# Kernel optimization log

Hardware: AMD Instinct MI355X
Metric: run time of the kernel (lower is better)

The kernel has to match this reference:

```python
import jax, jax.numpy as jnp
import numpy as np

B, N, C, H, W = 16, 10, 128, 48, 48

def setup_inputs() -> dict:
    key = jax.random.key(0)
    k0, k1 = jax.random.split(key, 2)
    x = jax.random.normal(k0, (B, N, C, H, W), dtype=jnp.float32)
    # trainable interpolation params, initialized to 0.5 as in the torch module
    pos_dec = jnp.full((N,), 0.5, dtype=jnp.float32)
    length_dec = jnp.full((N,), 0.5, dtype=jnp.float32)
    # 1x1 conv == channel-mixing matmul over N*C channels
    NC = N * C
    conv_w = jax.random.normal(k1, (NC, NC), dtype=jnp.float32) * (1.0 / np.sqrt(NC))
    conv_b = jnp.zeros((NC,), dtype=jnp.float32)
    return {"x": x, "pos_dec": pos_dec, "length_dec": length_dec,
            "conv_w": conv_w, "conv_b": conv_b}


def reference(x, pos_dec, length_dec, conv_w, conv_b):
    b, n, c, h, w = x.shape
    d = c * h * w
    q = x.reshape(b, n, d)          # proj_query (B,N,CHW)
    k = q                           # proj_key has the same flattened features
    # bi_interpolate with pos_int=i, length_int=1 reduces in closed form to:
    #   s0 = (1-pd)*K[i]   + pd*K[i+1]                      (key_short row)
    #   s1 = ld*((1-pd)*K[i+1] + pd*K[i+2])                 (zero-padded short mixed with key_long)
    # where indices wrap mod N (key was concatenated with itself).
    idx = jnp.arange(n)
    k1_ = k[:, (idx + 1) % n]       # (B,N,D)
    k2_ = k[:, (idx + 2) % n]
    pd = pos_dec[None, :, None]
    ld = length_dec[None, :, None]
    s0 = (1.0 - pd) * k + pd * k1_
    s1 = ld * ((1.0 - pd) * k1_ + pd * k2_)
    S = jnp.stack([s0, s1], axis=2)                 # (B,N,2,D) interpolated keys per group
    logits = jnp.einsum('bnd,bnkd->bnk', q, S)      # per-group 2-way attention scores
    attn = jax.nn.softmax(logits, axis=-1)          # softmax over the 2 searched keys
    out = jnp.einsum('bnk,bnkd->bnd', attn, S)      # (B,N,D)
    feat = out.reshape(b, n * c, h, w)
    conv = jnp.einsum('oc,bchw->bohw', conv_w, feat) + conv_b[None, :, None, None]
    return conv + x.reshape(b, n * c, h, w)
```

## Files before the change

kernel.cpp:

```cpp
#include <hip/hip_runtime.h>
#include <hip/hip_bf16.h>

#define BB 16
#define NN 10
#define CC 128
#define HWD 2304
#define DD (CC*HWD)
#define NC (NN*CC)

#define CHP 72

#define BM 256
#define BN 256
#define BK 64
#define TK (NC/BK)

typedef __bf16 bf16x8 __attribute__((ext_vector_type(8)));
typedef float  f32x4  __attribute__((ext_vector_type(4)));
typedef float  f32x16 __attribute__((ext_vector_type(16)));

#define XT_BYTES ((size_t)BB*HWD*NC*2)
#define W2_BYTES ((size_t)BB*NC*NC*2)
#define PART_FLOATS (BB*NN*CHP*3)
#define HEAD ((size_t)262144)

__device__ __forceinline__ ushort f2bf(float f) {
    __hip_bfloat16 h = __float2bfloat16(f);
    return *reinterpret_cast<ushort*>(&h);
}

__device__ __forceinline__ void gload_lds16(const ushort* g, ushort* l) {
    __builtin_amdgcn_global_load_lds(
        (const __attribute__((address_space(1))) void*)(const void*)g,
        (__attribute__((address_space(3))) void*)(void*)l,
        16, 0, 0);
}

__global__ __launch_bounds__(256) void k_trans(const float* __restrict__ x,
                                               ushort* __restrict__ xT,
                                               float* __restrict__ part) {
    __shared__ float tile[32*129];
    __shared__ float red[4][3];
    int hwt = blockIdx.x;
    int b   = blockIdx.y;
    int t = threadIdx.x;
    int hw0 = hwt*32;
    const float* xb = x + (size_t)b*NN*DD;

    int c_[4], ch_[4];
    size_t off_[4];
    #pragma unroll
    for (int i = 0; i < 4; ++i) {
        int s = i*256 + t;
        c_[i] = s >> 3; ch_[i] = s & 7;
        off_[i] = (size_t)c_[i]*HWD + hw0 + ch_[i]*4;
    }

    float4 s0[4], s1[4], s2[4], s3[4];
    #pragma unroll
    for (int i = 0; i < 4; ++i) s0[i] = *(const float4*)(xb + (size_t)0*DD + off_[i]);
    #pragma unroll
    for (int i = 0; i < 4; ++i) s1[i] = *(const float4*)(xb + (size_t)1*DD + off_[i]);
    #pragma unroll
    for (int i = 0; i < 4; ++i) s2[i] = *(const float4*)(xb + (size_t)2*DD + off_[i]);

    int w = t >> 6, l = t & 63;

    for (int n = 0; n < NN; ++n) {
        int n3 = (n + 3) % NN;
        #pragma unroll
        for (int i = 0; i < 4; ++i) s3[i] = *(const float4*)(xb + (size_t)n3*DD + off_[i]);

        float d0 = 0.f, d1 = 0.f, d2 = 0.f;
        #pragma unroll
        for (int i = 0; i < 4; ++i) {
            d0 += s0[i].x*s0[i].x + s0[i].y*s0[i].y + s0[i].z*s0[i].z + s0[i].w*s0[i].w;
            d1 += s0[i].x*s1[i].x + s0[i].y*s1[i].y + s0[i].z*s1[i].z + s0[i].w*s1[i].w;
            d2 += s0[i].x*s2[i].x + s0[i].y*s2[i].y + s0[i].z*s2[i].z + s0[i].w*s2[i].w;
        }
        for (int o = 32; o > 0; o >>= 1) {
            d0 += __shfl_down(d0, o);
            d1 += __shfl_down(d1, o);
            d2 += __shfl_down(d2, o);
        }
        if (l == 0) { red[w][0] = d0; red[w][1] = d1; red[w][2] = d2; }

        #pragma unroll
        for (int i = 0; i < 4; ++i) {
            int hwb = ch_[i]*4, cc = c_[i];
            tile[(hwb+0)*129 + cc] = s0[i].x;
            tile[(hwb+1)*129 + cc] = s0[i].y;
            tile[(hwb+2)*129 + cc] = s0[i].z;
            tile[(hwb+3)*129 + cc] = s0[i].w;
        }
        __syncthreads();

        if (t == 0) {
            float r0 = 0.f, r1 = 0.f, r2 = 0.f;
            #pragma unroll
            for (int i = 0; i < 4; ++i) { r0 += red[i][0]; r1 += red[i][1]; r2 += red[i][2]; }
            float* o = part + ((size_t)(b*NN + n)*CHP + hwt)*3;
            o[0] = r0; o[1] = r1; o[2] = r2;
        }

        int hwl = t >> 4;
        int cc0 = (t & 15) * 8;
        #pragma unroll
        for (int p = 0; p < 2; ++p) {
            int hw = p*16 + hwl;
            const float* src = &tile[hw*129 + cc0];
            union { ushort us[8]; uint4 v; } pk;
            #pragma unroll
            for (int j = 0; j < 8; ++j) pk.us[j] = f2bf(src[j]);
            ushort* dst = xT + (size_t)b*HWD*NC + (size_t)(hw0 + hw)*NC + n*CC + cc0;
            *(uint4*)dst = pk.v;
        }
        __syncthreads();
        #pragma unroll
        for (int i = 0; i < 4; ++i) { s0[i] = s1[i]; s1[i] = s2[i]; s2[i] = s3[i]; }
    }
}

__global__ void k_coef(const float* __restrict__ part,
                       const float* __restrict__ pos_dec,
                       const float* __restrict__ len_dec,
                       float* __restrict__ coef) {
    int bn = threadIdx.x;
    if (bn >= BB*NN) return;
    int n = bn % NN;
    float d0 = 0.f, d1 = 0.f, d2 = 0.f;
    const float* p = part + (size_t)bn*CHP*3;
    for (int i = 0; i < CHP; ++i) { d0 += p[i*3]; d1 += p[i*3+1]; d2 += p[i*3+2]; }
    float pd = pos_dec[n], ld = len_dec[n];
    float l0 = (1.f - pd)*d0 + pd*d1;
    float l1 = ld*((1.f - pd)*d1 + pd*d2);
    float m  = fmaxf(l0, l1);
    float e0 = expf(l0 - m), e1 = expf(l1 - m);
    float inv = 1.f/(e0 + e1);
    float a0 = e0*inv, a1 = e1*inv;
    coef[bn*3+0] = a0*(1.f - pd);
    coef[bn*3+1] = a0*pd + a1*ld*(1.f - pd);
    coef[bn*3+2] = a1*ld*pd;
}

__global__ __launch_bounds__(256) void k_w2(const float* __restrict__ w,
                                            const float* __restrict__ coef,
                                            ushort* __restrict__ w2) {
    int b = blockIdx.y;
    size_t eid = ((size_t)blockIdx.x*256 + threadIdx.x)*8;
    int o  = (int)(eid / NC);
    int mc = (int)(eid % NC);
    int m = mc >> 7, c = mc & 127;
    int m1 = (m + 9) % 10, m2 = (m + 8) % 10;
    float c0 = coef[(b*NN + m )*3 + 0];
    float c1 = coef[(b*NN + m1)*3 + 1];
    float c2 = coef[(b*NN + m2)*3 + 2];
    const float* wr = w + (size_t)o*NC;
    float4 a0 = *(const float4*)(wr + m *128 + c);
    float4 a1 = *(const float4*)(wr + m *128 + c + 4);
    float4 u0 = *(const float4*)(wr + m1*128 + c);
    float4 u1 = *(const float4*)(wr + m1*128 + c + 4);
    float4 v0 = *(const float4*)(wr + m2*128 + c);
    float4 v1 = *(const float4*)(wr + m2*128 + c + 4);
    union { ushort us[8]; uint4 v; } pk;
    pk.us[0] = f2bf(c0*a0.x + c1*u0.x + c2*v0.x);
    pk.us[1] = f2bf(c0*a0.y + c1*u0.y + c2*v0.y);
    pk.us[2] = f2bf(c0*a0.z + c1*u0.z + c2*v0.z);
    pk.us[3] = f2bf(c0*a0.w + c1*u0.w + c2*v0.w);
    pk.us[4] = f2bf(c0*a1.x + c1*u1.x + c2*v1.x);
    pk.us[5] = f2bf(c0*a1.y + c1*u1.y + c2*v1.y);
    pk.us[6] = f2bf(c0*a1.z + c1*u1.z + c2*v1.z);
    pk.us[7] = f2bf(c0*a1.w + c1*u1.w + c2*v1.w);
    *(uint4*)(w2 + (size_t)b*NC*NC + eid) = pk.v;
}

__global__ __launch_bounds__(256) void k_wconv(const float* __restrict__ w,
                                               ushort* __restrict__ wb) {
    int i = blockIdx.x*blockDim.x + threadIdx.x;
    size_t idx = (size_t)i*4;
    if (idx >= (size_t)NC*NC) return;
    float4 a = *(const float4*)(w + idx);
    ushort4 o;
    o.x = f2bf(a.x); o.y = f2bf(a.y); o.z = f2bf(a.z); o.w = f2bf(a.w);
    *(ushort4*)(wb + idx) = o;
}

__global__ __launch_bounds__(256) void k_feat(const float* __restrict__ x,
                                              const float* __restrict__ coef,
                                              ushort* __restrict__ featT) {
    __shared__ float tile[32*129];
    int hwt = blockIdx.x;
    int b   = blockIdx.y;
    int t = threadIdx.x;
    int hw0 = hwt*32;
    const float* xb = x + (size_t)b*NN*DD;

    int c_[4], ch_[4];
    size_t off_[4];
    #pragma unroll
    for (int i = 0; i < 4; ++i) {
        int s = i*256 + t;
        c_[i] = s >> 3; ch_[i] = s & 7;
        off_[i] = (size_t)c_[i]*HWD + hw0 + ch_[i]*4;
    }

    float4 s0[4], s1[4], s2[4], s3[4];
    #pragma unroll
    for (int i = 0; i < 4; ++i) s0[i] = *(const float4*)(xb + (size_t)0*DD + off_[i]);
    #pragma unroll
    for (int i = 0; i < 4; ++i) s1[i] = *(const float4*)(xb + (size_t)1*DD + off_[i]);
    #pragma unroll
    for (int i = 0; i < 4; ++i) s2[i] = *(const float4*)(xb + (size_t)2*DD + off_[i]);

    for (int n = 0; n < NN; ++n) {
        int n3 = (n + 3) % NN;
        #pragma unroll
        for (int i = 0; i < 4; ++i) s3[i] = *(const float4*)(xb + (size_t)n3*DD + off_[i]);

        int bn = b*NN + n;
        float c0 = coef[bn*3+0], c1 = coef[bn*3+1], c2 = coef[bn*3+2];

        #pragma unroll
        for (int i = 0; i < 4; ++i) {
            int hwb = ch_[i]*4, cc = c_[i];
            tile[(hwb+0)*129 + cc] = c0*s0[i].x + c1*s1[i].x + c2*s2[i].x;
            tile[(hwb+1)*129 + cc] = c0*s0[i].y + c1*s1[i].y + c2*s2[i].y;
            tile[(hwb+2)*129 + cc] = c0*s0[i].z + c1*s1[i].z + c2*s2[i].z;
            tile[(hwb+3)*129 + cc] = c0*s0[i].w + c1*s1[i].w + c2*s2[i].w;
        }
        __syncthreads();

        int hwl = t >> 4;
        int cc0 = (t & 15) * 8;
        #pragma unroll
        for (int p = 0; p < 2; ++p) {
            int hw = p*16 + hwl;
            const float* src = &tile[hw*129 + cc0];
            union { ushort us[8]; uint4 v; } pk;
            #pragma unroll
            for (int j = 0; j < 8; ++j) pk.us[j] = f2bf(src[j]);
            ushort* dst = featT + (size_t)b*HWD*NC + (size_t)(hw0 + hw)*NC + n*CC + cc0;
            *(uint4*)dst = pk.v;
        }
        __syncthreads();
        #pragma unroll
        for (int i = 0; i < 4; ++i) { s0[i] = s1[i]; s1[i] = s2[i]; s2[i] = s3[i]; }
    }
}

#define BAR()   __builtin_amdgcn_s_barrier()
#define SB()    __builtin_amdgcn_sched_barrier(0)
#define VM(N)   asm volatile("s_waitcnt vmcnt(" #N ")" ::: "memory")

__global__ __launch_bounds__(512, 2) void k_gemm(const ushort* __restrict__ Amat,
                                                 const ushort* __restrict__ Bmat,
                                                 const float* __restrict__ bias,
                                                 const float* __restrict__ x,
                                                 float* __restrict__ out,
                                                 size_t aStride) {
    __shared__ ushort L[2][4][BM*32];

    int bid = blockIdx.x;
    int wkid = (bid & 7) * 90 + (bid >> 3);
    int b   = wkid / 45;
    int r45 = wkid % 45;
    int hwt = r45 / 5;
    int ot  = r45 % 5;
    int o0 = ot*BM, hw0 = hwt*BN;

    int t = threadIdx.x;
    int l = t & 63;
    int w = t >> 6;
    int wr = w >> 2, wc = w & 3;

    const ushort* Ag = Amat + (size_t)b*aStride + (size_t)o0*NC;
    const ushort* Bg = Bmat + (size_t)b*HWD*NC + (size_t)hw0*NC;

    int r0 = t >> 2, c0 = t & 3;
    size_t g0 = (size_t)r0*NC + (size_t)((c0 ^ ((r0 >> 1) & 3)) * 8);
    size_t g1 = g0 + (size_t)128*NC;

#define STAGE(nb_, reg_, gp_) do { \
    gload_lds16((gp_) + g0, &L[nb_][reg_][t*8]); \
    gload_lds16((gp_) + g1, &L[nb_][reg_][(512 + t)*8]); } while (0)

    int fr32 = l & 31;
    int kh   = l >> 5;
    int sw   = (fr32 >> 1) & 3;
    int kcA  = ((kh)     ^ sw) << 3;
    int kcB  = ((2 | kh) ^ sw) << 3;
    int rA   = (wr*128 + fr32)*32;
    int rB   = (wc*64  + fr32)*32;

    f32x16 acc[4][2] = {};

#define COMP(Ar_, Br_) do { \
    bf16x8 a_[8], b0_, b1_, b2_, b3_; \
    _Pragma("unroll") \
    for (int mt = 0; mt < 4; ++mt) { \
        a_[mt*2+0] = *(const bf16x8*)&(Ar_)[rA + mt*1024 + kcA]; \
        a_[mt*2+1] = *(const bf16x8*)&(Ar_)[rA + mt*1024 + kcB]; \
    } \
    b0_ = *(const bf16x8*)&(Br_)[rB + kcA]; \
    b1_ = *(const bf16x8*)&(Br_)[rB + kcB]; \
    b2_ = *(const bf16x8*)&(Br_)[rB + 1024 + kcA]; \
    b3_ = *(const bf16x8*)&(Br_)[rB + 1024 + kcB]; \
    _Pragma("unroll") \
    for (int mt = 0; mt < 4; ++mt) { \
        acc[mt][0] = __builtin_amdgcn_mfma_f32_32x32x16_bf16(a_[mt*2+0], b0_, acc[mt][0], 0, 0, 0); \
        acc[mt][0] = __builtin_amdgcn_mfma_f32_32x32x16_bf16(a_[mt*2+1], b1_, acc[mt][0], 0, 0, 0); \
        acc[mt][1] = __builtin_amdgcn_mfma_f32_32x32x16_bf16(a_[mt*2+0], b2_, acc[mt][1], 0, 0, 0); \
        acc[mt][1] = __builtin_amdgcn_mfma_f32_32x32x16_bf16(a_[mt*2+1], b3_, acc[mt][1], 0, 0, 0); \
    } } while (0)

    STAGE(0, 0, Ag);
    STAGE(0, 2, Bg);
    STAGE(0, 1, Ag + 32);
    STAGE(0, 3, Bg + 32);
    VM(4);
    BAR();

    for (int kt = 0; kt < TK - 1; ++kt) {
        int buf = kt & 1, nbuf = buf ^ 1;
        const ushort* A0 = &L[buf][0][0];
        const ushort* A1 = &L[buf][1][0];
        const ushort* B0 = &L[buf][2][0];
        const ushort* B1 = &L[buf][3][0];
        const ushort* Agk = Ag + (size_t)(kt + 1)*BK;
        const ushort* Bgk = Bg + (size_t)(kt + 1)*BK;

        STAGE(nbuf, 0, Agk);
        STAGE(nbuf, 2, Bgk);
        SB();
        COMP(A0, B0);
        VM(4);
        BAR();

        STAGE(nbuf, 1, Agk + 32);
        STAGE(nbuf, 3, Bgk + 32);
        SB();
        COMP(A1, B1);
        VM(4);
        BAR();
    }

    {
        const int buf = (TK - 1) & 1;
        COMP((&L[buf][0][0]), (&L[buf][2][0]));
        VM(0);
        BAR();
        COMP((&L[buf][1][0]), (&L[buf][3][0]));
    }
#undef COMP
#undef STAGE

    #pragma unroll
    for (int mt = 0; mt < 4; ++mt) {
        #pragma unroll
        for (int nt = 0; nt < 2; ++nt) {
            int col = hw0 + wc*64 + nt*32 + fr32;
            #pragma unroll
            for (int reg = 0; reg < 16; ++reg) {
                int ro = o0 + wr*128 + mt*32 + (reg & 3) + 8*(reg >> 2) + 4*kh;
                size_t idx = (size_t)b*NC*HWD + (size_t)ro*HWD + col;
                out[idx] = acc[mt][nt][reg] + bias[ro] + x[idx];
            }
        }
    }
}

extern "C" void kernel_launch(void* const* d_in, const int* in_sizes, int n_in,
                              void* d_out, int out_size, void* d_ws, size_t ws_size,
                              hipStream_t stream) {
    const float* x       = (const float*)d_in[0];
    const float* pos_dec = (const float*)d_in[1];
    const float* len_dec = (const float*)d_in[2];
    const float* conv_w  = (const float*)d_in[3];
    const float* conv_b  = (const float*)d_in[4];
    float* out = (float*)d_out;

    char* ws = (char*)d_ws;
    float*  part = (float*)ws;
    float*  coef = part + PART_FLOATS;
    ushort* xT   = (ushort*)(ws + HEAD);

    k_trans<<<dim3(CHP, BB), 256, 0, stream>>>(x, xT, part);
    k_coef <<<dim3(1), 256, 0, stream>>>(part, pos_dec, len_dec, coef);

    if (ws_size >= HEAD + XT_BYTES + W2_BYTES) {
        ushort* w2 = (ushort*)(ws + HEAD + XT_BYTES);
        k_w2  <<<dim3(800, BB), 256, 0, stream>>>(conv_w, coef, w2);
        k_gemm<<<dim3(720), 512, 0, stream>>>(w2, xT, conv_b, x, out, (size_t)NC*NC);
    } else {
        ushort* wb = (ushort*)(ws + HEAD + XT_BYTES);
        k_wconv<<<dim3(1600), 256, 0, stream>>>(conv_w, wb);
        k_feat <<<dim3(CHP, BB), 256, 0, stream>>>(x, coef, xT);
        k_gemm <<<dim3(720), 512, 0, stream>>>(wb, xT, conv_b, x, out, (size_t)0);
    }
}
```

Measured before the change: 268.4 us.

## Replace two-buffer half-tile GEMM pipeline with four-slot ring prefetching three steps ahead

The GEMM main loop moves from a double buffer split into two K-halves to a four-slot LDS ring of 32-wide K tiles. Loads are issued three tiles ahead, and the wait keeps two tiles of global-to-LDS loads in flight instead of one. The goal is to hide more global memory latency behind MFMA work. LDS size is unchanged. The cost is one barrier per 32-wide K step, a drained tail of three compute steps, and more outstanding loads to track.

```diff
diff --git a/kernel.cpp b/kernel.cpp
--- a/kernel.cpp
+++ b/kernel.cpp
@@ -12,7 +12,7 @@
 
 #define BM 256
 #define BN 256
-#define BK 64
+#define BK 32
 #define TK (NC/BK)
 
 typedef __bf16 bf16x8 __attribute__((ext_vector_type(8)));
@@ -258,7 +258,7 @@
                                                  const float* __restrict__ x,
                                                  float* __restrict__ out,
                                                  size_t aStride) {
-    __shared__ ushort L[2][4][BM*32];
+    __shared__ ushort L[4][2][BM*BK];
 
     int bid = blockIdx.x;
     int wkid = (bid & 7) * 90 + (bid >> 3);
@@ -280,9 +280,12 @@
     size_t g0 = (size_t)r0*NC + (size_t)((c0 ^ ((r0 >> 1) & 3)) * 8);
     size_t g1 = g0 + (size_t)128*NC;
 
-#define STAGE(nb_, reg_, gp_) do { \
-    gload_lds16((gp_) + g0, &L[nb_][reg_][t*8]); \
-    gload_lds16((gp_) + g1, &L[nb_][reg_][(512 + t)*8]); } while (0)
+#define STAGE(sl_, kt_) do { \
+    size_t ko_ = (size_t)(kt_)*BK; \
+    gload_lds16(Ag + g0 + ko_, &L[sl_][0][t*8]); \
+    gload_lds16(Ag + g1 + ko_, &L[sl_][0][(512 + t)*8]); \
+    gload_lds16(Bg + g0 + ko_, &L[sl_][1][t*8]); \
+    gload_lds16(Bg + g1 + ko_, &L[sl_][1][(512 + t)*8]); } while (0)
 
     int fr32 = l & 31;
     int kh   = l >> 5;
@@ -294,17 +297,19 @@
 
     f32x16 acc[4][2] = {};
 
-#define COMP(Ar_, Br_) do { \
+#define COMP(sl_) do { \
+    const ushort* Ar_ = &L[sl_][0][0]; \
+    const ushort* Br_ = &L[sl_][1][0]; \
     bf16x8 a_[8], b0_, b1_, b2_, b3_; \
     _Pragma("unroll") \
     for (int mt = 0; mt < 4; ++mt) { \
-        a_[mt*2+0] = *(const bf16x8*)&(Ar_)[rA + mt*1024 + kcA]; \
-        a_[mt*2+1] = *(const bf16x8*)&(Ar_)[rA + mt*1024 + kcB]; \
+        a_[mt*2+0] = *(const bf16x8*)&Ar_[rA + mt*1024 + kcA]; \
+        a_[mt*2+1] = *(const bf16x8*)&Ar_[rA + mt*1024 + kcB]; \
     } \
-    b0_ = *(const bf16x8*)&(Br_)[rB + kcA]; \
-    b1_ = *(const bf16x8*)&(Br_)[rB + kcB]; \
-    b2_ = *(const bf16x8*)&(Br_)[rB + 1024 + kcA]; \
-    b3_ = *(const bf16x8*)&(Br_)[rB + 1024 + kcB]; \
+    b0_ = *(const bf16x8*)&Br_[rB + kcA]; \
+    b1_ = *(const bf16x8*)&Br_[rB + kcB]; \
+    b2_ = *(const bf16x8*)&Br_[rB + 1024 + kcA]; \
+    b3_ = *(const bf16x8*)&Br_[rB + 1024 + kcB]; \
     _Pragma("unroll") \
     for (int mt = 0; mt < 4; ++mt) { \
         acc[mt][0] = __builtin_amdgcn_mfma_f32_32x32x16_bf16(a_[mt*2+0], b0_, acc[mt][0], 0, 0, 0); \
@@ -313,44 +318,27 @@
         acc[mt][1] = __builtin_amdgcn_mfma_f32_32x32x16_bf16(a_[mt*2+1], b3_, acc[mt][1], 0, 0, 0); \
     } } while (0)
 
-    STAGE(0, 0, Ag);
-    STAGE(0, 2, Bg);
-    STAGE(0, 1, Ag + 32);
-    STAGE(0, 3, Bg + 32);
+    STAGE(0, 0);
+    STAGE(1, 1);
+    STAGE(2, 2);
+    VM(8);
+    BAR();
+
+    for (int kt = 0; kt < TK - 3; ++kt) {
+        STAGE((kt + 3) & 3, kt + 3);
+        SB();
+        COMP(kt & 3);
+        VM(8);
+        BAR();
+    }
+    COMP((TK - 3) & 3);
     VM(4);
     BAR();
-
-    for (int kt = 0; kt < TK - 1; ++kt) {
-        int buf = kt & 1, nbuf = buf ^ 1;
-        const ushort* A0 = &L[buf][0][0];
-        const ushort* A1 = &L[buf][1][0];
-        const ushort* B0 = &L[buf][2][0];
-        const ushort* B1 = &L[buf][3][0];
-        const ushort* Agk = Ag + (size_t)(kt + 1)*BK;
-        const ushort* Bgk = Bg + (size_t)(kt + 1)*BK;
-
-        STAGE(nbuf, 0, Agk);
-        STAGE(nbuf, 2, Bgk);
-        SB();
-        COMP(A0, B0);
-        VM(4);
-        BAR();
-
-        STAGE(nbuf, 1, Agk + 32);
-        STAGE(nbuf, 3, Bgk + 32);
-        SB();
-        COMP(A1, B1);
-        VM(4);
-        BAR();
-    }
-
-    {
-        const int buf = (TK - 1) & 1;
-        COMP((&L[buf][0][0]), (&L[buf][2][0]));
-        VM(0);
-        BAR();
-        COMP((&L[buf][1][0]), (&L[buf][3][0]));
-    }
+    COMP((TK - 2) & 3);
+    VM(0);
+    BAR();
+    COMP((TK - 1) & 3);
+
 #undef COMP
 #undef STAGE
 
```

New measurement: 273.4 us. No clear change (+1.9%).
